# Optimization experiments

Hardware: AMD Instinct MI355X
Metric: run time of the kernel (lower is better)

## Reference

```python
import jax, jax.numpy as jnp
import numpy as np

DIM = 1024
HEADS = 16


def setup_inputs() -> dict:
    key = jax.random.key(0)
    ks = jax.random.split(key, 9)
    B, N, C = 2, 2048, DIM
    hd = C // HEADS
    s = 1.0 / np.sqrt(C)
    x = jax.random.normal(ks[0], (B, N, C), dtype=jnp.float32)
    wq = jax.random.normal(ks[1], (C, C), dtype=jnp.float32) * s
    wk = jax.random.normal(ks[2], (C, C), dtype=jnp.float32) * s
    wv = jax.random.normal(ks[3], (C, C), dtype=jnp.float32) * s
    wp = jax.random.normal(ks[4], (C, C), dtype=jnp.float32) * s
    bp = jnp.zeros((C,), dtype=jnp.float32)
    # rotary table: angles theta_j = 10000^{-2j/hd}, positions 0..N-1
    inv_freq = 1.0 / (10000.0 ** (jnp.arange(0, hd, 2, dtype=jnp.float32) / hd))
    ang = jnp.arange(N, dtype=jnp.float32)[:, None] * inv_freq[None, :]  # (N, hd//2)
    cos = jnp.cos(ang)
    sin = jnp.sin(ang)
    return {"x": x, "wq": wq, "wk": wk, "wv": wv, "wp": wp, "bp": bp,
            "cos": cos, "sin": sin, "num_heads": HEADS}


def _apply_rotary(t, cos, sin):
    # t: (B, N, H, D); cos/sin: (N, D//2) -> broadcast (1, N, 1, D//2)
    B, N, H, D = t.shape
    tr = t.reshape(B, N, H, D // 2, 2)
    t1, t2 = tr[..., 0], tr[..., 1]
    c = cos[None, :, None, :]
    s = sin[None, :, None, :]
    o1 = t1 * c - t2 * s
    o2 = t1 * s + t2 * c
    return jnp.stack([o1, o2], axis=-1).reshape(B, N, H, D)


def reference(x, wq, wk, wv, wp, bp, cos, sin, num_heads):
    B, N, C = x.shape
    H = num_heads
    D = C // H
    q = (x @ wq.T).reshape(B, N, H, D)
    k = (x @ wk.T).reshape(B, N, H, D)
    v = (x @ wv.T).reshape(B, N, H, D)
    q = _apply_rotary(q, cos, sin)
    k = _apply_rotary(k, cos, sin)
    scale = 1.0 / jnp.sqrt(jnp.asarray(D, dtype=x.dtype))
    # scores: (B, H, N, N)
    scores = jnp.einsum('bnhd,bmhd->bhnm', q, k) * scale
    attn = jax.nn.softmax(scores, axis=-1)
    out = jnp.einsum('bhnm,bmhd->bnhd', attn, v).reshape(B, N, C)
    return out @ wp.T + bp
```

## Files before the change

kernel.cpp:

```cpp
#include <hip/hip_runtime.h>
#include <hip/hip_bf16.h>
#include <stdint.h>

#define DEVI __device__ __forceinline__

using bf16 = __hip_bfloat16;
typedef __bf16 bf16x8 __attribute__((ext_vector_type(8)));
typedef __bf16 bf16x4 __attribute__((ext_vector_type(4)));
typedef float f32x4 __attribute__((ext_vector_type(4)));
typedef float f32x16 __attribute__((ext_vector_type(16)));
typedef int i32x2 __attribute__((ext_vector_type(2)));

static constexpr int Bb = 2, Nn = 2048, Cc = 1024, Hh = 16, Dd = 64;
static constexpr float CSC = 0.125f * 1.44269504088896340736f;

DEVI bf16 f2bf(float x) {
  __bf16 h = (__bf16)x;
  return *(bf16*)&h;
}
DEVI float fexp2(float x) { return __builtin_amdgcn_exp2f(x); }

DEVI bf16x8 cvt8(f32x4 a, f32x4 b) {
  bf16x8 r;
  r[0] = (__bf16)a[0]; r[1] = (__bf16)a[1]; r[2] = (__bf16)a[2]; r[3] = (__bf16)a[3];
  r[4] = (__bf16)b[0]; r[5] = (__bf16)b[1]; r[6] = (__bf16)b[2]; r[7] = (__bf16)b[3];
  return r;
}

DEVI uint32_t pk2(float a, float b) {
  __bf16 x = (__bf16)a, y = (__bf16)b;
  uint16_t ux = *(uint16_t*)&x, uy = *(uint16_t*)&y;
  return (uint32_t)ux | ((uint32_t)uy << 16);
}

DEVI bf16x8 mk8(uint32_t a, uint32_t b, uint32_t c, uint32_t d) {
  union { uint32_t u[4]; bf16x8 v; } x;
  x.u[0] = a; x.u[1] = b; x.u[2] = c; x.u[3] = d;
  return x.v;
}

DEVI void gld_lds16(const bf16* g, bf16* l) {
  __builtin_amdgcn_global_load_lds(
      (__attribute__((address_space(1))) void*)(g),
      (__attribute__((address_space(3))) void*)(l),
      16, 0, 0);
}

__global__ __launch_bounds__(256) void k_cvt(const float* __restrict__ x,
                                             const float* __restrict__ wq,
                                             const float* __restrict__ wk,
                                             const float* __restrict__ wv,
                                             const float* __restrict__ wp,
                                             bf16* xb, bf16* wqb, bf16* wkb,
                                             bf16* wvb, bf16* wpb) {
  int bid = blockIdx.x;
  const float* src; bf16* dst; size_t off;
  if (bid < 2048) {
    src = x; dst = xb; off = (size_t)bid * 2048;
  } else {
    int s = (bid - 2048) >> 9, r = (bid - 2048) & 511;
    off = (size_t)r * 2048;
    src = s == 0 ? wq : s == 1 ? wk : s == 2 ? wv : wp;
    dst = s == 0 ? wqb : s == 1 ? wkb : s == 2 ? wvb : wpb;
  }
  size_t i = off + (size_t)threadIdx.x * 8;
  f32x4 a = *(const f32x4*)(src + i);
  f32x4 b = *(const f32x4*)(src + i + 4);
  *(bf16x8*)(dst + i) = cvt8(a, b);
}

template <int MFC, class Epi>
DEVI void gemm_dbuf(const bf16* __restrict__ A, const bf16* __restrict__ Bw,
                    int K, int m0, int n0, bf16* lA, bf16* lB, Epi epi) {
  constexpr int BM = MFC * 32;
  constexpr int PA = BM / 64;
  constexpr int ASZ = BM * 32, BSZ = 128 * 32;
  const int t = threadIdx.x;
  const int lane = t & 63, wave = t >> 6, g = lane >> 4;
  const int wr = wave >> 1, wc = wave & 1;

  auto stage = [&](int k0, int buf) {
#pragma unroll
    for (int p = 0; p < PA; ++p) {
      int c = p * 256 + t;
      gld_lds16(A + (size_t)(m0 + (c >> 2)) * K + k0 + (c & 3) * 8,
                lA + buf * ASZ + (size_t)(p * 256 + wave * 64) * 8);
    }
#pragma unroll
    for (int p = 0; p < 2; ++p) {
      int c = p * 256 + t;
      gld_lds16(Bw + (size_t)(n0 + (c >> 2)) * K + k0 + (c & 3) * 8,
                lB + buf * BSZ + (size_t)(p * 256 + wave * 64) * 8);
    }
  };

  f32x4 acc[MFC][4] = {};
  stage(0, 0);
  __syncthreads();

  const int NS = K / 32;
  for (int s = 0; s < NS; ++s) {
    const int cur = s & 1;
    if (s + 1 < NS) stage((s + 1) * 32, cur ^ 1);

    bf16x8 aF[MFC];
#pragma unroll
    for (int mf = 0; mf < MFC; ++mf)
      aF[mf] = *(const bf16x8*)(lA + cur * ASZ +
                                (wr * (BM / 2) + mf * 16 + (lane & 15)) * 32 + g * 8);
#pragma unroll
    for (int nf = 0; nf < 4; ++nf) {
      bf16x8 bF = *(const bf16x8*)(lB + cur * BSZ +
                                   (wc * 64 + nf * 16 + (lane & 15)) * 32 + g * 8);
#pragma unroll
      for (int mf = 0; mf < MFC; ++mf)
        acc[mf][nf] = __builtin_amdgcn_mfma_f32_16x16x32_bf16(aF[mf], bF, acc[mf][nf], 0, 0, 0);
    }
    __syncthreads();
  }

#pragma unroll
  for (int mf = 0; mf < MFC; ++mf)
#pragma unroll
    for (int nf = 0; nf < 4; ++nf)
#pragma unroll
      for (int r = 0; r < 4; ++r) {
        int gm = m0 + wr * (BM / 2) + mf * 16 + g * 4 + r;
        int gn = n0 + wc * 64 + nf * 16 + (lane & 15);
        epi(gm, gn, acc[mf][nf][r]);
      }
}

struct EpiRope {
  bf16* dst; const float* cosw; const float* sinw; float scale;
  DEVI void operator()(int gm, int gn, float v) const {
    int b = gm >> 11, n = gm & 2047;
    int h = gn >> 6, d = gn & 63;
    int i = d >> 1;
    float c = cosw[n * 32 + i], s = sinw[n * 32 + i];
    float p = __shfl_xor(v, 1);
    float o = (d & 1) ? (p * s + v * c) : (v * c - p * s);
    dst[((size_t)(b * Hh + h) * Nn + n) * 64 + d] = f2bf(o * scale);
  }
};

struct EpiVt {
  bf16* dst;
  DEVI void operator()(int gm, int gn, float v) const {
    int h = gm >> 6, d = gm & 63;
    int b = gn >> 11, n = gn & 2047;
    dst[((size_t)(b * Hh + h) * 64 + d) * Nn + n] = f2bf(v);
  }
};

struct EpiProj {
  float* dst; const float* bias;
  DEVI void operator()(int gm, int gn, float v) const {
    dst[(size_t)gm * Cc + gn] = v + bias[gn];
  }
};

__global__ __launch_bounds__(256) void k_qkv(const bf16* __restrict__ xb,
                                             const bf16* __restrict__ wqb,
                                             const bf16* __restrict__ wkb,
                                             const bf16* __restrict__ wvb,
                                             bf16* q_ws, bf16* k_ws, bf16* vt_ws,
                                             const float* __restrict__ cw,
                                             const float* __restrict__ sw) {
  __shared__ __align__(16) bf16 lA[2 * 128 * 32];
  __shared__ __align__(16) bf16 lB[2 * 128 * 32];
  int bid = blockIdx.x;
  if (bid < 512) {
    int sub = bid & 255;
    int m0 = (sub >> 3) * 128, n0 = (sub & 7) * 128;
    bool isq = bid < 256;
    gemm_dbuf<4>(xb, isq ? wqb : wkb, Cc, m0, n0, lA, lB,
                 EpiRope{isq ? q_ws : k_ws, cw, sw, isq ? CSC : 1.0f});
  } else {
    int sub = bid - 512;
    int m0 = (sub & 7) * 128, n0 = (sub >> 3) * 128;
    gemm_dbuf<4>(wvb, xb, Cc, m0, n0, lA, lB, EpiVt{vt_ws});
  }
}

__global__ __launch_bounds__(256) void k_proj(const bf16* __restrict__ A,
                                              const bf16* __restrict__ W,
                                              float* dst, const float* __restrict__ bias) {
  __shared__ __align__(16) bf16 lA[2 * 64 * 32];
  __shared__ __align__(16) bf16 lB[2 * 128 * 32];
  gemm_dbuf<2>(A, W, Cc, blockIdx.x * 64, blockIdx.y * 128, lA, lB,
               EpiProj{dst, bias});
}

__global__ __launch_bounds__(256) void k_flash(const bf16* __restrict__ q_ws,
                                               const bf16* __restrict__ k_ws,
                                               const bf16* __restrict__ vt_ws,
                                               bf16* __restrict__ attn_o) {
  __shared__ __align__(16) bf16 lK[2][64 * 64];
  __shared__ __align__(16) bf16 lV[2][64 * 64];

  const int t = threadIdx.x, lane = t & 63, wave = t >> 6;
  const int l31 = lane & 31, hi = lane >> 5;
  const int bh = blockIdx.y;
  const int q0w = blockIdx.x * 128 + wave * 32;
  const bf16* qg = q_ws + (size_t)bh * Nn * 64;
  const bf16* kg = k_ws + (size_t)bh * Nn * 64;
  const bf16* vg = vt_ws + (size_t)bh * 64 * Nn;

  bf16x8 qF[4];
#pragma unroll
  for (int kd = 0; kd < 4; ++kd)
    qF[kd] = *(const bf16x8*)(qg + (size_t)(q0w + l31) * 64 + kd * 16 + hi * 8);

  f32x16 accO[2] = {};
  float LsL = 0.f;

  auto stage_tile = [&](int kt, int buf) {
#pragma unroll
    for (int p = 0; p < 2; ++p) {
      int c = p * 256 + t;
      int row = c >> 3, cis = (c & 7) ^ (row & 7);
      gld_lds16(kg + (size_t)(kt * 64 + row) * 64 + cis * 8,
                lK[buf] + (size_t)(p * 256 + wave * 64) * 8);
      gld_lds16(vg + (size_t)row * Nn + kt * 64 + cis * 8,
                lV[buf] + (size_t)(p * 256 + wave * 64) * 8);
    }
  };

  stage_tile(0, 0);
  __syncthreads();

  constexpr int NT = Nn / 64;
  for (int kt = 0; kt < NT; ++kt) {
    const int cur = kt & 1;
    if (kt + 1 < NT) stage_tile(kt + 1, cur ^ 1);

#pragma unroll
    for (int kb = 0; kb < 2; ++kb) {
      f32x16 accT = {};
      __builtin_amdgcn_s_setprio(1);
#pragma unroll
      for (int kd = 0; kd < 4; ++kd) {
        int row = kb * 32 + l31;
        bf16x8 kF = *(const bf16x8*)(lK[cur] +
            ((row * 64 + kd * 16 + hi * 8) ^ ((row & 7) << 3)));
        accT = __builtin_amdgcn_mfma_f32_32x32x16_bf16(kF, qF[kd], accT, 0, 0, 0);
      }
      __builtin_amdgcn_s_setprio(0);

      float p[16];
#pragma unroll
      for (int r = 0; r < 16; ++r) { p[r] = fexp2(accT[r]); LsL += p[r]; }

      uint32_t c01 = pk2(p[0], p[1]),  c23 = pk2(p[2], p[3]);
      uint32_t c89 = pk2(p[4], p[5]),  cab = pk2(p[6], p[7]);
      uint32_t d01 = pk2(p[8], p[9]),  d23 = pk2(p[10], p[11]);
      uint32_t d89 = pk2(p[12], p[13]), dab = pk2(p[14], p[15]);
      i32x2 s0a = __builtin_amdgcn_permlane32_swap((int)c01, (int)c89, false, false);
      i32x2 s0b = __builtin_amdgcn_permlane32_swap((int)c23, (int)cab, false, false);
      i32x2 s1a = __builtin_amdgcn_permlane32_swap((int)d01, (int)d89, false, false);
      i32x2 s1b = __builtin_amdgcn_permlane32_swap((int)d23, (int)dab, false, false);
      bf16x8 paF[2] = { mk8(s0a[0], s0b[0], s0a[1], s0b[1]),
                        mk8(s1a[0], s1b[0], s1a[1], s1b[1]) };

      __builtin_amdgcn_s_setprio(1);
#pragma unroll
      for (int d0 = 0; d0 < 2; ++d0) {
#pragma unroll
        for (int s = 0; s < 2; ++s) {
          int vrow = d0 * 32 + l31;
          bf16x8 vF = *(const bf16x8*)(lV[cur] +
              ((vrow * 64 + kb * 32 + s * 16 + hi * 8) ^ ((vrow & 7) << 3)));
          accO[d0] = __builtin_amdgcn_mfma_f32_32x32x16_bf16(paF[s], vF, accO[d0], 0, 0, 0);
        }
      }
      __builtin_amdgcn_s_setprio(0);
    }

    __syncthreads();
  }

  float L = LsL + __shfl_xor(LsL, 32);

  const int b = bh >> 4, h = bh & 15;
#pragma unroll
  for (int r = 0; r < 16; ++r) {
    int ql = (r & 3) + 8 * (r >> 2) + 4 * hi;
    float inv = 1.0f / __shfl(L, ql);
    int qrow = q0w + ql;
#pragma unroll
    for (int d0 = 0; d0 < 2; ++d0) {
      int d = d0 * 32 + l31;
      attn_o[((size_t)(b * Nn + qrow)) * Cc + h * 64 + d] = f2bf(accO[d0][r] * inv);
    }
  }
}

extern "C" void kernel_launch(void* const* d_in, const int* in_sizes, int n_in,
                              void* d_out, int out_size, void* d_ws, size_t ws_size,
                              hipStream_t stream) {
  (void)in_sizes; (void)n_in; (void)out_size; (void)ws_size;
  const float* x  = (const float*)d_in[0];
  const float* wq = (const float*)d_in[1];
  const float* wk = (const float*)d_in[2];
  const float* wv = (const float*)d_in[3];
  const float* wp = (const float*)d_in[4];
  const float* bp = (const float*)d_in[5];
  const float* cw = (const float*)d_in[6];
  const float* sw = (const float*)d_in[7];
  float* out = (float*)d_out;

  const size_t M1 = 1u << 20;
  bf16* x_bf  = (bf16*)d_ws;
  bf16* wq_bf = x_bf + 4 * M1;
  bf16* wk_bf = wq_bf + M1;
  bf16* wv_bf = wk_bf + M1;
  bf16* wp_bf = wv_bf + M1;
  bf16* q_ws  = wp_bf + M1;
  bf16* k_ws  = q_ws + 4 * M1;
  bf16* vt_ws = k_ws + 4 * M1;
  bf16* ao_ws = x_bf;

  k_cvt  <<<dim3(4096),    dim3(256), 0, stream>>>(x, wq, wk, wv, wp,
                                                   x_bf, wq_bf, wk_bf, wv_bf, wp_bf);
  k_qkv  <<<dim3(768),     dim3(256), 0, stream>>>(x_bf, wq_bf, wk_bf, wv_bf,
                                                   q_ws, k_ws, vt_ws, cw, sw);
  k_flash<<<dim3(16, 32),  dim3(256), 0, stream>>>(q_ws, k_ws, vt_ws, ao_ws);
  k_proj <<<dim3(64, 8),   dim3(256), 0, stream>>>(ao_ws, wp_bf, out, bp);
}
```

Baseline: 132.6 us.

## Triple-buffer LDS staging in GEMM and flash kernels with explicit vmcnt waits

```diff
diff --git a/kernel.cpp b/kernel.cpp
--- a/kernel.cpp
+++ b/kernel.cpp
@@ -6,7 +6,6 @@
 
 using bf16 = __hip_bfloat16;
 typedef __bf16 bf16x8 __attribute__((ext_vector_type(8)));
-typedef __bf16 bf16x4 __attribute__((ext_vector_type(4)));
 typedef float f32x4 __attribute__((ext_vector_type(4)));
 typedef float f32x16 __attribute__((ext_vector_type(16)));
 typedef int i32x2 __attribute__((ext_vector_type(2)));
@@ -14,10 +13,7 @@
 static constexpr int Bb = 2, Nn = 2048, Cc = 1024, Hh = 16, Dd = 64;
 static constexpr float CSC = 0.125f * 1.44269504088896340736f;
 
-DEVI bf16 f2bf(float x) {
-  __bf16 h = (__bf16)x;
-  return *(bf16*)&h;
-}
+DEVI bf16 f2bf(float x) { __bf16 h = (__bf16)x; return *(bf16*)&h; }
 DEVI float fexp2(float x) { return __builtin_amdgcn_exp2f(x); }
 
 DEVI bf16x8 cvt8(f32x4 a, f32x4 b) {
@@ -44,6 +40,17 @@
       (__attribute__((address_space(1))) void*)(g),
       (__attribute__((address_space(3))) void*)(l),
       16, 0, 0);
+}
+
+template <int N>
+DEVI void wait_vm() {
+  if constexpr (N == 0)      asm volatile("s_waitcnt vmcnt(0)" ::: "memory");
+  else if constexpr (N == 3) asm volatile("s_waitcnt vmcnt(3)" ::: "memory");
+  else                       asm volatile("s_waitcnt vmcnt(4)" ::: "memory");
+}
+DEVI void barrier_raw() {
+  __builtin_amdgcn_s_barrier();
+  __builtin_amdgcn_sched_barrier(0);
 }
 
 __global__ __launch_bounds__(256) void k_cvt(const float* __restrict__ x,
@@ -74,6 +81,7 @@
                     int K, int m0, int n0, bf16* lA, bf16* lB, Epi epi) {
   constexpr int BM = MFC * 32;
   constexpr int PA = BM / 64;
+  constexpr int NLD = PA + 2;
   constexpr int ASZ = BM * 32, BSZ = 128 * 32;
   const int t = threadIdx.x;
   const int lane = t & 63, wave = t >> 6, g = lane >> 4;
@@ -96,12 +104,14 @@
 
   f32x4 acc[MFC][4] = {};
   stage(0, 0);
-  __syncthreads();
+  stage(32, 1);
+  wait_vm<NLD>();
+  barrier_raw();
 
   const int NS = K / 32;
+  int cur = 0;
   for (int s = 0; s < NS; ++s) {
-    const int cur = s & 1;
-    if (s + 1 < NS) stage((s + 1) * 32, cur ^ 1);
+    if (s + 2 < NS) stage((s + 2) * 32, (cur + 2) % 3);
 
     bf16x8 aF[MFC];
 #pragma unroll
@@ -116,7 +126,11 @@
       for (int mf = 0; mf < MFC; ++mf)
         acc[mf][nf] = __builtin_amdgcn_mfma_f32_16x16x32_bf16(aF[mf], bF, acc[mf][nf], 0, 0, 0);
     }
-    __syncthreads();
+
+    if (s + 2 < NS)      wait_vm<NLD>();
+    else if (s + 1 < NS) wait_vm<0>();
+    barrier_raw();
+    cur = (cur + 1) % 3;
   }
 
 #pragma unroll
@@ -167,8 +181,8 @@
                                              bf16* q_ws, bf16* k_ws, bf16* vt_ws,
                                              const float* __restrict__ cw,
                                              const float* __restrict__ sw) {
-  __shared__ __align__(16) bf16 lA[2 * 128 * 32];
-  __shared__ __align__(16) bf16 lB[2 * 128 * 32];
+  __shared__ __align__(16) bf16 lA[3 * 128 * 32];
+  __shared__ __align__(16) bf16 lB[3 * 128 * 32];
   int bid = blockIdx.x;
   if (bid < 512) {
     int sub = bid & 255;
@@ -186,8 +200,8 @@
 __global__ __launch_bounds__(256) void k_proj(const bf16* __restrict__ A,
                                               const bf16* __restrict__ W,
                                               float* dst, const float* __restrict__ bias) {
-  __shared__ __align__(16) bf16 lA[2 * 64 * 32];
-  __shared__ __align__(16) bf16 lB[2 * 128 * 32];
+  __shared__ __align__(16) bf16 lA[3 * 64 * 32];
+  __shared__ __align__(16) bf16 lB[3 * 128 * 32];
   gemm_dbuf<2>(A, W, Cc, blockIdx.x * 64, blockIdx.y * 128, lA, lB,
                EpiProj{dst, bias});
 }
@@ -196,8 +210,8 @@
                                                const bf16* __restrict__ k_ws,
                                                const bf16* __restrict__ vt_ws,
                                                bf16* __restrict__ attn_o) {
-  __shared__ __align__(16) bf16 lK[2][64 * 64];
-  __shared__ __align__(16) bf16 lV[2][64 * 64];
+  __shared__ __align__(16) bf16 lK[3][64 * 64];
+  __shared__ __align__(16) bf16 lV[3][64 * 64];
 
   const int t = threadIdx.x, lane = t & 63, wave = t >> 6;
   const int l31 = lane & 31, hi = lane >> 5;
@@ -228,12 +242,14 @@
   };
 
   stage_tile(0, 0);
-  __syncthreads();
+  stage_tile(1, 1);
+  wait_vm<4>();
+  barrier_raw();
 
   constexpr int NT = Nn / 64;
+  int cur = 0;
   for (int kt = 0; kt < NT; ++kt) {
-    const int cur = kt & 1;
-    if (kt + 1 < NT) stage_tile(kt + 1, cur ^ 1);
+    if (kt + 2 < NT) stage_tile(kt + 2, (cur + 2) % 3);
 
 #pragma unroll
     for (int kb = 0; kb < 2; ++kb) {
@@ -277,7 +293,10 @@
       __builtin_amdgcn_s_setprio(0);
     }
 
-    __syncthreads();
+    if (kt + 2 < NT)      wait_vm<4>();
+    else if (kt + 1 < NT) wait_vm<0>();
+    barrier_raw();
+    cur = (cur + 1) % 3;
   }
 
   float L = LsL + __shfl_xor(LsL, 32);
```

New measurement: 145.7 us. 9.9% more time.

## Load K/V fragments straight to registers in flash kernel, drop LDS and barriers

Applied to the files above, without the earlier changes.

```diff
diff --git a/kernel.cpp b/kernel.cpp
--- a/kernel.cpp
+++ b/kernel.cpp
@@ -6,7 +6,6 @@
 
 using bf16 = __hip_bfloat16;
 typedef __bf16 bf16x8 __attribute__((ext_vector_type(8)));
-typedef __bf16 bf16x4 __attribute__((ext_vector_type(4)));
 typedef float f32x4 __attribute__((ext_vector_type(4)));
 typedef float f32x16 __attribute__((ext_vector_type(16)));
 typedef int i32x2 __attribute__((ext_vector_type(2)));
@@ -14,10 +13,7 @@
 static constexpr int Bb = 2, Nn = 2048, Cc = 1024, Hh = 16, Dd = 64;
 static constexpr float CSC = 0.125f * 1.44269504088896340736f;
 
-DEVI bf16 f2bf(float x) {
-  __bf16 h = (__bf16)x;
-  return *(bf16*)&h;
-}
+DEVI bf16 f2bf(float x) { __bf16 h = (__bf16)x; return *(bf16*)&h; }
 DEVI float fexp2(float x) { return __builtin_amdgcn_exp2f(x); }
 
 DEVI bf16x8 cvt8(f32x4 a, f32x4 b) {
@@ -192,17 +188,19 @@
                EpiProj{dst, bias});
 }
 
-__global__ __launch_bounds__(256) void k_flash(const bf16* __restrict__ q_ws,
-                                               const bf16* __restrict__ k_ws,
-                                               const bf16* __restrict__ vt_ws,
-                                               bf16* __restrict__ attn_o) {
-  __shared__ __align__(16) bf16 lK[2][64 * 64];
-  __shared__ __align__(16) bf16 lV[2][64 * 64];
-
+__global__ __launch_bounds__(256, 2) void k_flash(const bf16* __restrict__ q_ws,
+                                                  const bf16* __restrict__ k_ws,
+                                                  const bf16* __restrict__ vt_ws,
+                                                  bf16* __restrict__ attn_o) {
   const int t = threadIdx.x, lane = t & 63, wave = t >> 6;
   const int l31 = lane & 31, hi = lane >> 5;
-  const int bh = blockIdx.y;
-  const int q0w = blockIdx.x * 128 + wave * 32;
+
+  const int bid = blockIdx.x;
+  const int slot = bid >> 3;
+  const int bh = (bid & 7) * 4 + (slot >> 4);
+  const int qx = slot & 15;
+  const int q0w = qx * 128 + wave * 32;
+
   const bf16* qg = q_ws + (size_t)bh * Nn * 64;
   const bf16* kg = k_ws + (size_t)bh * Nn * 64;
   const bf16* vg = vt_ws + (size_t)bh * 64 * Nn;
@@ -215,37 +213,33 @@
   f32x16 accO[2] = {};
   float LsL = 0.f;
 
-  auto stage_tile = [&](int kt, int buf) {
-#pragma unroll
-    for (int p = 0; p < 2; ++p) {
-      int c = p * 256 + t;
-      int row = c >> 3, cis = (c & 7) ^ (row & 7);
-      gld_lds16(kg + (size_t)(kt * 64 + row) * 64 + cis * 8,
-                lK[buf] + (size_t)(p * 256 + wave * 64) * 8);
-      gld_lds16(vg + (size_t)row * Nn + kt * 64 + cis * 8,
-                lV[buf] + (size_t)(p * 256 + wave * 64) * 8);
-    }
+  auto loadK = [&](int kt, bf16x8 (&kF)[8]) {
+#pragma unroll
+    for (int kb = 0; kb < 2; ++kb)
+#pragma unroll
+      for (int kd = 0; kd < 4; ++kd)
+        kF[kb * 4 + kd] = *(const bf16x8*)(kg +
+            (size_t)(kt * 64 + kb * 32 + l31) * 64 + kd * 16 + hi * 8);
   };
-
-  stage_tile(0, 0);
-  __syncthreads();
-
-  constexpr int NT = Nn / 64;
-  for (int kt = 0; kt < NT; ++kt) {
-    const int cur = kt & 1;
-    if (kt + 1 < NT) stage_tile(kt + 1, cur ^ 1);
-
+  auto loadV = [&](int kt, bf16x8 (&vF)[8]) {
+#pragma unroll
+    for (int d0 = 0; d0 < 2; ++d0)
+#pragma unroll
+      for (int kb = 0; kb < 2; ++kb)
+#pragma unroll
+        for (int s = 0; s < 2; ++s)
+          vF[d0 * 4 + kb * 2 + s] = *(const bf16x8*)(vg +
+              (size_t)(d0 * 32 + l31) * Nn + kt * 64 + kb * 32 + s * 16 + hi * 8);
+  };
+
+  auto compute = [&](const bf16x8 (&kF)[8], const bf16x8 (&vF)[8]) {
 #pragma unroll
     for (int kb = 0; kb < 2; ++kb) {
       f32x16 accT = {};
       __builtin_amdgcn_s_setprio(1);
 #pragma unroll
-      for (int kd = 0; kd < 4; ++kd) {
-        int row = kb * 32 + l31;
-        bf16x8 kF = *(const bf16x8*)(lK[cur] +
-            ((row * 64 + kd * 16 + hi * 8) ^ ((row & 7) << 3)));
-        accT = __builtin_amdgcn_mfma_f32_32x32x16_bf16(kF, qF[kd], accT, 0, 0, 0);
-      }
+      for (int kd = 0; kd < 4; ++kd)
+        accT = __builtin_amdgcn_mfma_f32_32x32x16_bf16(kF[kb * 4 + kd], qF[kd], accT, 0, 0, 0);
       __builtin_amdgcn_s_setprio(0);
 
       float p[16];
@@ -258,26 +252,32 @@
       uint32_t d89 = pk2(p[12], p[13]), dab = pk2(p[14], p[15]);
       i32x2 s0a = __builtin_amdgcn_permlane32_swap((int)c01, (int)c89, false, false);
       i32x2 s0b = __builtin_amdgcn_permlane32_swap((int)c23, (int)cab, false, false);
-      i32x2 s1a = __builtin_amdgcn_permlane32_swap((int)d01, (int)d89, false, false);
-      i32x2 s1b = __builtin_amdgcn_permlane32_swap((int)d23, (int)dab, false, false);
+      i32x2 s1a = __builtin_amdgcn_permlane32_swap((int)d01, (int)d23, false, false);
+      i32x2 s1b = __builtin_amdgcn_permlane32_swap((int)d89, (int)dab, false, false);
+      (void)s1a; (void)s1b;
+      i32x2 t1a = __builtin_amdgcn_permlane32_swap((int)d01, (int)d89, false, false);
+      i32x2 t1b = __builtin_amdgcn_permlane32_swap((int)d23, (int)dab, false, false);
       bf16x8 paF[2] = { mk8(s0a[0], s0b[0], s0a[1], s0b[1]),
-                        mk8(s1a[0], s1b[0], s1a[1], s1b[1]) };
+                        mk8(t1a[0], t1b[0], t1a[1], t1b[1]) };
 
       __builtin_amdgcn_s_setprio(1);
 #pragma unroll
-      for (int d0 = 0; d0 < 2; ++d0) {
-#pragma unroll
-        for (int s = 0; s < 2; ++s) {
-          int vrow = d0 * 32 + l31;
-          bf16x8 vF = *(const bf16x8*)(lV[cur] +
-              ((vrow * 64 + kb * 32 + s * 16 + hi * 8) ^ ((vrow & 7) << 3)));
-          accO[d0] = __builtin_amdgcn_mfma_f32_32x32x16_bf16(paF[s], vF, accO[d0], 0, 0, 0);
-        }
-      }
+      for (int d0 = 0; d0 < 2; ++d0)
+#pragma unroll
+        for (int s = 0; s < 2; ++s)
+          accO[d0] = __builtin_amdgcn_mfma_f32_32x32x16_bf16(paF[s], vF[d0 * 4 + kb * 2 + s], accO[d0], 0, 0, 0);
       __builtin_amdgcn_s_setprio(0);
     }
-
-    __syncthreads();
+  };
+
+  constexpr int NT = Nn / 64;
+  bf16x8 kA[8], vA[8], kB[8], vB[8];
+  loadK(0, kA); loadV(0, vA);
+  for (int kt = 0; kt < NT; kt += 2) {
+    if (kt + 1 < NT) { loadK(kt + 1, kB); loadV(kt + 1, vB); }
+    compute(kA, vA);
+    if (kt + 2 < NT) { loadK(kt + 2, kA); loadV(kt + 2, vA); }
+    if (kt + 1 < NT) compute(kB, vB);
   }
 
   float L = LsL + __shfl_xor(LsL, 32);
@@ -325,6 +325,6 @@
                                                    x_bf, wq_bf, wk_bf, wv_bf, wp_bf);
   k_qkv  <<<dim3(768),     dim3(256), 0, stream>>>(x_bf, wq_bf, wk_bf, wv_bf,
                                                    q_ws, k_ws, vt_ws, cw, sw);
-  k_flash<<<dim3(16, 32),  dim3(256), 0, stream>>>(q_ws, k_ws, vt_ws, ao_ws);
+  k_flash<<<dim3(512),     dim3(256), 0, stream>>>(q_ws, k_ws, vt_ws, ao_ws);
   k_proj <<<dim3(64, 8),   dim3(256), 0, stream>>>(ao_ws, wp_bf, out, bp);
 }
```

New measurement: 193.8 us. 1.46x slower.
